# Kernel tuning notes

Measured on AMD Instinct MI355X. Metric: run time of the kernel, lower is better.

## Reference

```python
import jax, jax.numpy as jnp
import numpy as np

N_NODES = 50000
N_EDGES = 1_600_000
IN_DIM = 64
HID_DIM = 64
OUT_DIM = 64


def setup_inputs() -> dict:
    key = jax.random.key(0)
    k = jax.random.split(key, 7)
    feat = jax.random.normal(k[0], (N_NODES, IN_DIM), dtype=jnp.float32)
    src = jax.random.randint(k[1], (N_EDGES,), 0, N_NODES, dtype=jnp.int32)
    dst = jax.random.randint(k[2], (N_EDGES,), 0, N_NODES, dtype=jnp.int32)
    # nn.init.normal_(weight, std=0.1); bias default uniform ~ small, use 0.1*randn
    W1 = 0.1 * jax.random.normal(k[3], (HID_DIM, IN_DIM), dtype=jnp.float32)
    b1 = 0.1 * jax.random.normal(k[4], (HID_DIM,), dtype=jnp.float32)
    W2 = 0.1 * jax.random.normal(k[5], (OUT_DIM, HID_DIM), dtype=jnp.float32)
    b2 = 0.1 * jax.random.normal(k[6], (OUT_DIM,), dtype=jnp.float32)
    return {"feat": feat, "src": src, "dst": dst, "W1": W1, "b1": b1, "W2": W2, "b2": b2}


def _gnn_layer(h, src, dst, W, b):
    # copy_u + sum: gather source-node features along edges, scatter-sum to dst
    agg = jax.ops.segment_sum(h[src], dst, num_segments=N_NODES)  # [N, d_in]
    return agg @ W.T + b  # nn.Linear


def reference(feat, src, dst, W1, b1, W2, b2):
    h = _gnn_layer(feat, src, dst, W1, b1)
    h = jnp.tanh(h)
    h = _gnn_layer(h, src, dst, W2, b2)
    return h
```

## Files before the change

kernel.cpp:

```cpp
#include <hip/hip_runtime.h>

#define N_NODES 50000
#define N_EDGES 1600000
#define DIM 64
#define NBK 196
#define BIN_BLOCKS 391
#define CSR_CAP 12288
#define QCAP 3072
#define GEMM_BLOCKS 197
#define NB_AGG 12500

__device__ __forceinline__ unsigned short f2bf(float f) {
    union { float f; unsigned u; } v; v.f = f;
    unsigned r = v.u + 0x7FFF + ((v.u >> 16) & 1);
    return (unsigned short)(r >> 16);
}
__device__ __forceinline__ float bf2f(unsigned short h) {
    union { unsigned u; float f; } v; v.u = ((unsigned)h) << 16;  return v.f;
}

__global__ __launch_bounds__(256) void bin_and_gemm1(const int* __restrict__ src,
                                                     const int* __restrict__ dst,
                                                     int* __restrict__ bcur,
                                                     int* __restrict__ binned,
                                                     const float* __restrict__ X,
                                                     const float* __restrict__ W,
                                                     unsigned short* __restrict__ T) {
    __shared__ int cnt[NBK];
    __shared__ int lofs[NBK];
    __shared__ int shiftv[NBK];
    __shared__ int sb[256];
    __shared__ int stag[4096];
    __shared__ unsigned char stb[4096];
    __shared__ float Ws[64 * 64];
    int tid = threadIdx.x;

    if (blockIdx.x >= BIN_BLOCKS) {
#pragma unroll
        for (int j = 0; j < 16; ++j) Ws[j * 256 + tid] = W[j * 256 + tid];
        __syncthreads();

        int n = (blockIdx.x - BIN_BLOCKS) * 256 + tid;
        if (n > N_NODES) return;
        ushort4* tp = (ushort4*)(T + (size_t)n * 64);
        if (n == N_NODES) {
            ushort4 z = {0, 0, 0, 0};
#pragma unroll
            for (int k = 0; k < 16; ++k) tp[k] = z;
            return;
        }

        float4 x[16];
        const float4* xp = (const float4*)(X + (size_t)n * 64);
#pragma unroll
        for (int k = 0; k < 16; ++k) x[k] = xp[k];

        for (int fg = 0; fg < 16; ++fg) {
            float r[4];
#pragma unroll
            for (int fi = 0; fi < 4; ++fi) {
                int f = fg * 4 + fi;
                float acc = 0.f;
#pragma unroll
                for (int k4 = 0; k4 < 16; ++k4) {
                    float4 w = *(const float4*)&Ws[f * 64 + k4 * 4];
                    float4 xv = x[k4];
                    acc += xv.x * w.x + xv.y * w.y + xv.z * w.z + xv.w * w.w;
                }
                r[fi] = acc;
            }
            ushort4 o;
            o.x = f2bf(r[0]); o.y = f2bf(r[1]); o.z = f2bf(r[2]); o.w = f2bf(r[3]);
            tp[fg] = o;
        }
        return;
    }

    if (tid < NBK) cnt[tid] = 0;
    __syncthreads();

    int base = blockIdx.x * 4096;
    int nedge = N_EDGES - base;
    if (nedge > 4096) nedge = 4096;

    int myb[16], myr[16], myp[16];
#pragma unroll
    for (int i = 0; i < 16; ++i) {
        int e = base + i * 256 + tid;
        myb[i] = -1;
        if (e < N_EDGES) {
            int s = src[e], d = dst[e];
            int b = d >> 8;
            myb[i] = b;
            myp[i] = ((d & 255) << 16) | s;
            myr[i] = atomicAdd(&cnt[b], 1);
        }
    }
    __syncthreads();

    int c = (tid < NBK) ? cnt[tid] : 0;
    sb[tid] = c;
    __syncthreads();
    for (int off = 1; off < 256; off <<= 1) {
        int u = (tid >= off) ? sb[tid - off] : 0;
        __syncthreads();
        sb[tid] += u;
        __syncthreads();
    }
    if (tid < NBK) {
        lofs[tid] = sb[tid] - c;
        if (c) shiftv[tid] = tid * CSR_CAP + atomicAdd(&bcur[tid * 16], c) - lofs[tid];
    }
    __syncthreads();

#pragma unroll
    for (int i = 0; i < 16; ++i) {
        if (myb[i] >= 0) {
            int idx = lofs[myb[i]] + myr[i];
            stag[idx] = myp[i];
            stb[idx] = (unsigned char)myb[i];
        }
    }
    __syncthreads();

    for (int i = tid; i < nedge; i += 256)
        binned[i + shiftv[stb[i]]] = stag[i];
}

__global__ __launch_bounds__(256) void build_csr(const int* __restrict__ binned,
                                                 const int* __restrict__ bcur,
                                                 unsigned* __restrict__ nodeinfo,
                                                 unsigned short* __restrict__ csr16) {
    __shared__ int cnt[64], cnt2[64], ofs[64], sb[64];
    __shared__ int qtot;
    int tid = threadIdx.x;
    int b = blockIdx.x >> 2;
    int q = blockIdx.x & 3;
    int ibase = b * CSR_CAP;
    int qbase = (b * 4 + q) * QCAP;
    int m = bcur[b * 16];
    if (m > CSR_CAP) m = CSR_CAP;
    if (tid < 64) { cnt[tid] = 0; cnt2[tid] = 0; }
    __syncthreads();

    for (int i = tid; i < m; i += 256) {
        int dl = (binned[ibase + i] >> 16) & 255;
        if ((dl >> 6) == q) atomicAdd(&cnt[dl & 63], 1);
    }
    __syncthreads();

    int v = 0;
    if (tid < 64) { v = (cnt[tid] + 15) & ~15; sb[tid] = v; }
    __syncthreads();
    for (int off = 1; off < 64; off <<= 1) {
        int u = (tid >= off && tid < 64) ? sb[tid - off] : 0;
        __syncthreads();
        if (tid < 64) sb[tid] += u;
        __syncthreads();
    }
    if (tid < 64) {
        ofs[tid] = sb[tid] - v;
        int node = (b << 8) + (q << 6) + tid;
        if (node < N_NODES)
            nodeinfo[node] = ((unsigned)v << 23) | (unsigned)(qbase + ofs[tid]);
    }
    if (tid == 63) qtot = sb[63];
    __syncthreads();

    int qt = qtot;
    for (int i = tid; i < qt; i += 256) csr16[qbase + i] = (unsigned short)N_NODES;
    __syncthreads();

    for (int i = tid; i < m; i += 256) {
        int p = binned[ibase + i];
        int dl = (p >> 16) & 255;
        if ((dl >> 6) == q) {
            int r = atomicAdd(&cnt2[dl & 63], 1);
            csr16[qbase + ofs[dl & 63] + r] = (unsigned short)(p & 0xFFFF);
        }
    }
}

__global__ __launch_bounds__(256) void agg_fuse1(const unsigned short* __restrict__ T,
                                                 const unsigned short* __restrict__ csr,
                                                 const unsigned* __restrict__ nodeinfo,
                                                 const float* __restrict__ b1,
                                                 const float* __restrict__ W2,
                                                 unsigned short* __restrict__ T2) {
    __shared__ float4 W2t4[1024];
    __shared__ float hsf[4 * 64];
    int tid = threadIdx.x;
    int w = tid >> 6;
    int lane = tid & 63;
    int node = blockIdx.x * 4 + w;

    for (int L4 = tid; L4 < 1024; L4 += 256) {
        int k4 = L4 >> 6, f = L4 & 63;
        W2t4[L4] = *(const float4*)(W2 + f * 64 + k4 * 4);
    }

    unsigned info = nodeinfo[node];
    int pos = (int)(info & 0x7FFFFFu);
    int groups = (int)(info >> 23) >> 3;
    const uint4* ix = (const uint4*)(csr + pos);
    float acc = b1[lane];
    float acc2 = 0.f;
    for (int g = 0; g < groups; g += 2) {
        uint4 ia = ix[g];
        uint4 ib = ix[g + 1];
        int s0 = ia.x & 0xFFFF, s1 = ia.x >> 16;
        int s2 = ia.y & 0xFFFF, s3 = ia.y >> 16;
        int s4 = ia.z & 0xFFFF, s5 = ia.z >> 16;
        int s6 = ia.w & 0xFFFF, s7 = ia.w >> 16;
        int u0 = ib.x & 0xFFFF, u1 = ib.x >> 16;
        int u2 = ib.y & 0xFFFF, u3 = ib.y >> 16;
        int u4 = ib.z & 0xFFFF, u5 = ib.z >> 16;
        int u6 = ib.w & 0xFFFF, u7 = ib.w >> 16;
        unsigned short v0 = T[(size_t)s0 * DIM + lane];
        unsigned short v1 = T[(size_t)s1 * DIM + lane];
        unsigned short v2 = T[(size_t)s2 * DIM + lane];
        unsigned short v3 = T[(size_t)s3 * DIM + lane];
        unsigned short v4 = T[(size_t)s4 * DIM + lane];
        unsigned short v5 = T[(size_t)s5 * DIM + lane];
        unsigned short v6 = T[(size_t)s6 * DIM + lane];
        unsigned short v7 = T[(size_t)s7 * DIM + lane];
        unsigned short w0 = T[(size_t)u0 * DIM + lane];
        unsigned short w1 = T[(size_t)u1 * DIM + lane];
        unsigned short w2 = T[(size_t)u2 * DIM + lane];
        unsigned short w3 = T[(size_t)u3 * DIM + lane];
        unsigned short w4 = T[(size_t)u4 * DIM + lane];
        unsigned short w5 = T[(size_t)u5 * DIM + lane];
        unsigned short w6 = T[(size_t)u6 * DIM + lane];
        unsigned short w7 = T[(size_t)u7 * DIM + lane];
        acc  += (bf2f(v0) + bf2f(v1)) + (bf2f(v2) + bf2f(v3)) +
                (bf2f(v4) + bf2f(v5)) + (bf2f(v6) + bf2f(v7));
        acc2 += (bf2f(w0) + bf2f(w1)) + (bf2f(w2) + bf2f(w3)) +
                (bf2f(w4) + bf2f(w5)) + (bf2f(w6) + bf2f(w7));
    }
    acc += acc2;

    float e = __expf(2.f * acc);
    hsf[w * 64 + lane] = 1.f - 2.f / (e + 1.f);
    __syncthreads();

    const float4* hv4 = (const float4*)&hsf[w * 64];
    float tf = 0.f;
#pragma unroll
    for (int k4 = 0; k4 < 16; ++k4) {
        float4 hv = hv4[k4];
        float4 wv = W2t4[k4 * 64 + lane];
        tf += hv.x * wv.x + hv.y * wv.y + hv.z * wv.z + hv.w * wv.w;
    }
    T2[(size_t)node * DIM + lane] = f2bf(tf);

    if (blockIdx.x == 0 && tid < 64)
        T2[(size_t)N_NODES * DIM + tid] = 0;
}

__global__ __launch_bounds__(256) void agg_out(const unsigned short* __restrict__ T,
                                               const unsigned short* __restrict__ csr,
                                               const unsigned* __restrict__ nodeinfo,
                                               const float* __restrict__ bias,
                                               float* __restrict__ outp) {
    int node = blockIdx.x * 4 + (threadIdx.x >> 6);
    int lane = threadIdx.x & 63;
    if (node >= N_NODES) return;
    unsigned info = nodeinfo[node];
    int pos = (int)(info & 0x7FFFFFu);
    int groups = (int)(info >> 23) >> 3;
    const uint4* ix = (const uint4*)(csr + pos);
    float acc = bias[lane];
    float acc2 = 0.f;
    for (int g = 0; g < groups; g += 2) {
        uint4 ia = ix[g];
        uint4 ib = ix[g + 1];
        int s0 = ia.x & 0xFFFF, s1 = ia.x >> 16;
        int s2 = ia.y & 0xFFFF, s3 = ia.y >> 16;
        int s4 = ia.z & 0xFFFF, s5 = ia.z >> 16;
        int s6 = ia.w & 0xFFFF, s7 = ia.w >> 16;
        int u0 = ib.x & 0xFFFF, u1 = ib.x >> 16;
        int u2 = ib.y & 0xFFFF, u3 = ib.y >> 16;
        int u4 = ib.z & 0xFFFF, u5 = ib.z >> 16;
        int u6 = ib.w & 0xFFFF, u7 = ib.w >> 16;
        unsigned short v0 = T[(size_t)s0 * DIM + lane];
        unsigned short v1 = T[(size_t)s1 * DIM + lane];
        unsigned short v2 = T[(size_t)s2 * DIM + lane];
        unsigned short v3 = T[(size_t)s3 * DIM + lane];
        unsigned short v4 = T[(size_t)s4 * DIM + lane];
        unsigned short v5 = T[(size_t)s5 * DIM + lane];
        unsigned short v6 = T[(size_t)s6 * DIM + lane];
        unsigned short v7 = T[(size_t)s7 * DIM + lane];
        unsigned short w0 = T[(size_t)u0 * DIM + lane];
        unsigned short w1 = T[(size_t)u1 * DIM + lane];
        unsigned short w2 = T[(size_t)u2 * DIM + lane];
        unsigned short w3 = T[(size_t)u3 * DIM + lane];
        unsigned short w4 = T[(size_t)u4 * DIM + lane];
        unsigned short w5 = T[(size_t)u5 * DIM + lane];
        unsigned short w6 = T[(size_t)u6 * DIM + lane];
        unsigned short w7 = T[(size_t)u7 * DIM + lane];
        acc  += (bf2f(v0) + bf2f(v1)) + (bf2f(v2) + bf2f(v3)) +
                (bf2f(v4) + bf2f(v5)) + (bf2f(v6) + bf2f(v7));
        acc2 += (bf2f(w0) + bf2f(w1)) + (bf2f(w2) + bf2f(w3)) +
                (bf2f(w4) + bf2f(w5)) + (bf2f(w6) + bf2f(w7));
    }
    acc += acc2;
    outp[(size_t)node * DIM + lane] = acc;
}

extern "C" void kernel_launch(void* const* d_in, const int* in_sizes, int n_in,
                              void* d_out, int out_size, void* d_ws, size_t ws_size,
                              hipStream_t stream) {
    const float* feat = (const float*)d_in[0];
    const int*   src  = (const int*)d_in[1];
    const int*   dst  = (const int*)d_in[2];
    const float* W1   = (const float*)d_in[3];
    const float* b1   = (const float*)d_in[4];
    const float* W2   = (const float*)d_in[5];
    const float* b2   = (const float*)d_in[6];
    float* out = (float*)d_out;

    int*            binned   = (int*)d_ws;
    unsigned short* csr16    = (unsigned short*)(binned + NBK * CSR_CAP);
    unsigned*       nodeinfo = (unsigned*)(csr16 + NBK * 4 * QCAP);
    int*            bcur     = (int*)(nodeinfo + N_NODES);
    unsigned short* t        = (unsigned short*)(bcur + NBK * 16 + 8);
    unsigned short* t2       = t + (size_t)(N_NODES + 1) * 64;

    hipMemsetAsync(bcur, 0, NBK * 16 * sizeof(int), stream);
    bin_and_gemm1<<<BIN_BLOCKS + GEMM_BLOCKS, 256, 0, stream>>>(
        src, dst, bcur, binned, feat, W1, t);
    build_csr<<<NBK * 4, 256, 0, stream>>>(binned, bcur, nodeinfo, csr16);

    agg_fuse1<<<NB_AGG, 256, 0, stream>>>(t, csr16, nodeinfo, b1, W2, t2);

    agg_out<<<NB_AGG, 256, 0, stream>>>(t2, csr16, nodeinfo, b2, out);
}
```

Before: 234.2 us.

## Gather neighbor rows as 16-byte vectors with edge-parallel sub-groups and LDS reduction

Both aggregation kernels now split each 64-lane wave into 8 groups of 8 lanes. Each group handles one edge per chunk and each lane loads 16 bytes (8 bf16 features) of the source row, replacing one 2-byte load per lane per edge. Partial sums from the 8 groups go into shared memory and are reduced per feature after a barrier. This cuts the number of memory instructions per edge and reads whole rows in wide transactions. The cost is more registers, an added LDS stage and block-wide sync, and agg_out drops its node bounds check.

Result: no change. 236.7 us (+1.1%).

```diff
diff --git a/kernel.cpp b/kernel.cpp
--- a/kernel.cpp
+++ b/kernel.cpp
@@ -17,6 +17,12 @@
 }
 __device__ __forceinline__ float bf2f(unsigned short h) {
     union { unsigned u; float f; } v; v.u = ((unsigned)h) << 16;  return v.f;
+}
+__device__ __forceinline__ float blo(unsigned u) {
+    union { unsigned u; float f; } v; v.u = u << 16; return v.f;
+}
+__device__ __forceinline__ float bhi(unsigned u) {
+    union { unsigned u; float f; } v; v.u = u & 0xFFFF0000u; return v.f;
 }
 
 __global__ __launch_bounds__(256) void bin_and_gemm1(const int* __restrict__ src,
@@ -188,10 +194,13 @@
                                                  const float* __restrict__ W2,
                                                  unsigned short* __restrict__ T2) {
     __shared__ float4 W2t4[1024];
+    __shared__ float part[4][8][64];
     __shared__ float hsf[4 * 64];
     int tid = threadIdx.x;
     int w = tid >> 6;
     int lane = tid & 63;
+    int g8 = lane >> 3;
+    int fs = lane & 7;
     int node = blockIdx.x * 4 + w;
 
     for (int L4 = tid; L4 < 1024; L4 += 256) {
@@ -201,43 +210,34 @@
 
     unsigned info = nodeinfo[node];
     int pos = (int)(info & 0x7FFFFFu);
-    int groups = (int)(info >> 23) >> 3;
-    const uint4* ix = (const uint4*)(csr + pos);
+    int nch = (int)(info >> 23) >> 3;
+    const unsigned short* ip = csr + pos + g8;
+    const uint4* Tp = (const uint4*)T;
+    float a0 = 0.f, a1 = 0.f, a2 = 0.f, a3 = 0.f, a4 = 0.f, a5 = 0.f, a6 = 0.f, a7 = 0.f;
+    float c0 = 0.f, c1 = 0.f, c2 = 0.f, c3 = 0.f, c4 = 0.f, c5 = 0.f, c6 = 0.f, c7 = 0.f;
+    for (int c = 0; c < nch; c += 2) {
+        int i0 = ip[c * 8];
+        int i1 = ip[c * 8 + 8];
+        uint4 da = Tp[(size_t)i0 * 8 + fs];
+        uint4 db = Tp[(size_t)i1 * 8 + fs];
+        a0 += blo(da.x); a1 += bhi(da.x);
+        a2 += blo(da.y); a3 += bhi(da.y);
+        a4 += blo(da.z); a5 += bhi(da.z);
+        a6 += blo(da.w); a7 += bhi(da.w);
+        c0 += blo(db.x); c1 += bhi(db.x);
+        c2 += blo(db.y); c3 += bhi(db.y);
+        c4 += blo(db.z); c5 += bhi(db.z);
+        c6 += blo(db.w); c7 += bhi(db.w);
+    }
+    float4 pa = {a0 + c0, a1 + c1, a2 + c2, a3 + c3};
+    float4 pb = {a4 + c4, a5 + c5, a6 + c6, a7 + c7};
+    *(float4*)&part[w][g8][fs * 8] = pa;
+    *(float4*)&part[w][g8][fs * 8 + 4] = pb;
+    __syncthreads();
+
     float acc = b1[lane];
-    float acc2 = 0.f;
-    for (int g = 0; g < groups; g += 2) {
-        uint4 ia = ix[g];
-        uint4 ib = ix[g + 1];
-        int s0 = ia.x & 0xFFFF, s1 = ia.x >> 16;
-        int s2 = ia.y & 0xFFFF, s3 = ia.y >> 16;
-        int s4 = ia.z & 0xFFFF, s5 = ia.z >> 16;
-        int s6 = ia.w & 0xFFFF, s7 = ia.w >> 16;
-        int u0 = ib.x & 0xFFFF, u1 = ib.x >> 16;
-        int u2 = ib.y & 0xFFFF, u3 = ib.y >> 16;
-        int u4 = ib.z & 0xFFFF, u5 = ib.z >> 16;
-        int u6 = ib.w & 0xFFFF, u7 = ib.w >> 16;
-        unsigned short v0 = T[(size_t)s0 * DIM + lane];
-        unsigned short v1 = T[(size_t)s1 * DIM + lane];
-        unsigned short v2 = T[(size_t)s2 * DIM + lane];
-        unsigned short v3 = T[(size_t)s3 * DIM + lane];
-        unsigned short v4 = T[(size_t)s4 * DIM + lane];
-        unsigned short v5 = T[(size_t)s5 * DIM + lane];
-        unsigned short v6 = T[(size_t)s6 * DIM + lane];
-        unsigned short v7 = T[(size_t)s7 * DIM + lane];
-        unsigned short w0 = T[(size_t)u0 * DIM + lane];
-        unsigned short w1 = T[(size_t)u1 * DIM + lane];
-        unsigned short w2 = T[(size_t)u2 * DIM + lane];
-        unsigned short w3 = T[(size_t)u3 * DIM + lane];
-        unsigned short w4 = T[(size_t)u4 * DIM + lane];
-        unsigned short w5 = T[(size_t)u5 * DIM + lane];
-        unsigned short w6 = T[(size_t)u6 * DIM + lane];
-        unsigned short w7 = T[(size_t)u7 * DIM + lane];
-        acc  += (bf2f(v0) + bf2f(v1)) + (bf2f(v2) + bf2f(v3)) +
-                (bf2f(v4) + bf2f(v5)) + (bf2f(v6) + bf2f(v7));
-        acc2 += (bf2f(w0) + bf2f(w1)) + (bf2f(w2) + bf2f(w3)) +
-                (bf2f(w4) + bf2f(w5)) + (bf2f(w6) + bf2f(w7));
-    }
-    acc += acc2;
+#pragma unroll
+    for (int g = 0; g < 8; ++g) acc += part[w][g][lane];
 
     float e = __expf(2.f * acc);
     hsf[w * 64 + lane] = 1.f - 2.f / (e + 1.f);
@@ -262,48 +262,44 @@
                                                const unsigned* __restrict__ nodeinfo,
                                                const float* __restrict__ bias,
                                                float* __restrict__ outp) {
-    int node = blockIdx.x * 4 + (threadIdx.x >> 6);
-    int lane = threadIdx.x & 63;
-    if (node >= N_NODES) return;
+    __shared__ float part[4][8][64];
+    int tid = threadIdx.x;
+    int w = tid >> 6;
+    int lane = tid & 63;
+    int g8 = lane >> 3;
+    int fs = lane & 7;
+    int node = blockIdx.x * 4 + w;
+
     unsigned info = nodeinfo[node];
     int pos = (int)(info & 0x7FFFFFu);
-    int groups = (int)(info >> 23) >> 3;
-    const uint4* ix = (const uint4*)(csr + pos);
+    int nch = (int)(info >> 23) >> 3;
+    const unsigned short* ip = csr + pos + g8;
+    const uint4* Tp = (const uint4*)T;
+    float a0 = 0.f, a1 = 0.f, a2 = 0.f, a3 = 0.f, a4 = 0.f, a5 = 0.f, a6 = 0.f, a7 = 0.f;
+    float c0 = 0.f, c1 = 0.f, c2 = 0.f, c3 = 0.f, c4 = 0.f, c5 = 0.f, c6 = 0.f, c7 = 0.f;
+    for (int c = 0; c < nch; c += 2) {
+        int i0 = ip[c * 8];
+        int i1 = ip[c * 8 + 8];
+        uint4 da = Tp[(size_t)i0 * 8 + fs];
+        uint4 db = Tp[(size_t)i1 * 8 + fs];
+        a0 += blo(da.x); a1 += bhi(da.x);
+        a2 += blo(da.y); a3 += bhi(da.y);
+        a4 += blo(da.z); a5 += bhi(da.z);
+        a6 += blo(da.w); a7 += bhi(da.w);
+        c0 += blo(db.x); c1 += bhi(db.x);
+        c2 += blo(db.y); c3 += bhi(db.y);
+        c4 += blo(db.z); c5 += bhi(db.z);
+        c6 += blo(db.w); c7 += bhi(db.w);
+    }
+    float4 pa = {a0 + c0, a1 + c1, a2 + c2, a3 + c3};
+    float4 pb = {a4 + c4, a5 + c5, a6 + c6, a7 + c7};
+    *(float4*)&part[w][g8][fs * 8] = pa;
+    *(float4*)&part[w][g8][fs * 8 + 4] = pb;
+    __syncthreads();
+
     float acc = bias[lane];
-    float acc2 = 0.f;
-    for (int g = 0; g < groups; g += 2) {
-        uint4 ia = ix[g];
-        uint4 ib = ix[g + 1];
-        int s0 = ia.x & 0xFFFF, s1 = ia.x >> 16;
-        int s2 = ia.y & 0xFFFF, s3 = ia.y >> 16;
-        int s4 = ia.z & 0xFFFF, s5 = ia.z >> 16;
-        int s6 = ia.w & 0xFFFF, s7 = ia.w >> 16;
-        int u0 = ib.x & 0xFFFF, u1 = ib.x >> 16;
-        int u2 = ib.y & 0xFFFF, u3 = ib.y >> 16;
-        int u4 = ib.z & 0xFFFF, u5 = ib.z >> 16;
-        int u6 = ib.w & 0xFFFF, u7 = ib.w >> 16;
-        unsigned short v0 = T[(size_t)s0 * DIM + lane];
-        unsigned short v1 = T[(size_t)s1 * DIM + lane];
-        unsigned short v2 = T[(size_t)s2 * DIM + lane];
-        unsigned short v3 = T[(size_t)s3 * DIM + lane];
-        unsigned short v4 = T[(size_t)s4 * DIM + lane];
-        unsigned short v5 = T[(size_t)s5 * DIM + lane];
-        unsigned short v6 = T[(size_t)s6 * DIM + lane];
-        unsigned short v7 = T[(size_t)s7 * DIM + lane];
-        unsigned short w0 = T[(size_t)u0 * DIM + lane];
-        unsigned short w1 = T[(size_t)u1 * DIM + lane];
-        unsigned short w2 = T[(size_t)u2 * DIM + lane];
-        unsigned short w3 = T[(size_t)u3 * DIM + lane];
-        unsigned short w4 = T[(size_t)u4 * DIM + lane];
-        unsigned short w5 = T[(size_t)u5 * DIM + lane];
-        unsigned short w6 = T[(size_t)u6 * DIM + lane];
-        unsigned short w7 = T[(size_t)u7 * DIM + lane];
-        acc  += (bf2f(v0) + bf2f(v1)) + (bf2f(v2) + bf2f(v3)) +
-                (bf2f(v4) + bf2f(v5)) + (bf2f(v6) + bf2f(v7));
-        acc2 += (bf2f(w0) + bf2f(w1)) + (bf2f(w2) + bf2f(w3)) +
-                (bf2f(w4) + bf2f(w5)) + (bf2f(w6) + bf2f(w7));
-    }
-    acc += acc2;
+#pragma unroll
+    for (int g = 0; g < 8; ++g) acc += part[w][g][lane];
     outp[(size_t)node * DIM + lane] = acc;
 }
 
```
